# Performance work log

Measured on AMD Instinct MI355X. Metric: run time of the kernel, lower is better.

The kernel has to match this reference:

```python
import jax, jax.numpy as jnp
import numpy as np

B, NX, NY, NZ, C, MAX_PTS = 4, 512, 512, 1, 64, 32
P_PER_B = 16384            # non-empty pillars per frame (unique cells)
MASK_RATIO = 0.7


def setup_inputs() -> dict:
    key = jax.random.key(0)
    kf, kn, ks, kc = jax.random.split(key, 4)
    grid = NZ * NX * NY
    # unique linear pillar locations per batch element -> deterministic scatter-set
    lin = jnp.stack([
        jax.random.permutation(jax.random.fold_in(kc, b), grid)[:P_PER_B]
        for b in range(B)
    ])  # [B, P]
    y = (lin // NX).reshape(-1)
    x = (lin % NX).reshape(-1)
    bidx = jnp.repeat(jnp.arange(B), P_PER_B)
    voxel_coords = jnp.stack(
        [bidx, jnp.zeros_like(bidx), y, x], axis=1).astype(jnp.int32)  # [M,4] = (b,z,y,x)
    M = B * P_PER_B
    pillar_features = jax.random.normal(kf, (M, C), dtype=jnp.float32)
    voxel_num_points = jax.random.randint(kn, (M,), 1, MAX_PTS + 1, dtype=jnp.int32)
    K = int(M * (1.0 - MASK_RATIO))
    select_index = jnp.sort(jax.random.permutation(ks, M)[:K]).astype(jnp.int32)
    return {
        "pillar_features": pillar_features,
        "voxel_coords": voxel_coords,
        "voxel_num_points": voxel_num_points,
        "select_index": select_index,
    }


def reference(pillar_features, voxel_coords, voxel_num_points, select_index):
    grid = NZ * NX * NY
    # per-pillar flat index into the batched dense grid:
    # within-frame index = z + y*nx + x (nz == 1), offset by batch*grid
    flat = (voxel_coords[:, 0] * grid
            + voxel_coords[:, 1]
            + voxel_coords[:, 2] * NX
            + voxel_coords[:, 3])  # [M]

    fdt = pillar_features.dtype
    occupancy = jnp.zeros(B * grid, dtype=fdt).at[flat].set(1.0).reshape(B, NY, NX)
    points_number = (jnp.zeros(B * grid, dtype=voxel_num_points.dtype)
                     .at[flat].set(voxel_num_points).reshape(B, NY, NX))
    density = (jnp.zeros(B * grid, dtype=fdt)
               .at[flat].set(voxel_num_points.astype(fdt) / MAX_PTS)
               .reshape(B, NY, NX))

    # scatter only the unmasked (selected) pillar features into the dense BEV grid
    flat_sel = flat[select_index]               # [K]
    feats_sel = pillar_features[select_index]   # [K, C]
    spatial = (jnp.zeros((B * grid, C), dtype=fdt)
               .at[flat_sel].set(feats_sel)
               .reshape(B, grid, C)
               .transpose(0, 2, 1)
               .reshape(B, C * NZ, NY, NX))
    return spatial, occupancy, density, points_number
```

## Files before the change

kernel.cpp:

```cpp
#include <hip/hip_runtime.h>

#define NXD   512
#define NYD   512
#define CD    64
#define BD    4
#define GRIDC (NXD * NYD)

__global__ void scatter_meta_kernel(const int* __restrict__ coords,
                                    const int* __restrict__ npts,
                                    float* __restrict__ occ,
                                    float* __restrict__ dens,
                                    float* __restrict__ pnum,
                                    int M) {
    int i = blockIdx.x * blockDim.x + threadIdx.x;
    if (i >= M) return;
    int b = coords[4 * i + 0];
    int z = coords[4 * i + 1];
    int y = coords[4 * i + 2];
    int x = coords[4 * i + 3];
    int cell = b * GRIDC + z + y * NXD + x;
    float n = (float)npts[i];
    occ[cell]  = 1.0f;
    dens[cell] = n * (1.0f / 32.0f);
    pnum[cell] = n;
}

__global__ void scatter_spatial_kernel(const float* __restrict__ feats,
                                       const int* __restrict__ coords,
                                       const int* __restrict__ sel,
                                       float* __restrict__ spatial,
                                       int K) {
    int group = blockIdx.x * (blockDim.x >> 6) + (threadIdx.x >> 6);
    int c     = threadIdx.x & 63;
    if (group >= K) return;
    int row = sel[group];
    int b = coords[4 * row + 0];
    int z = coords[4 * row + 1];
    int y = coords[4 * row + 2];
    int x = coords[4 * row + 3];
    int cell = z + y * NXD + x;
    float v = feats[(size_t)row * CD + c];
    spatial[(size_t)b * ((size_t)CD * GRIDC) + (size_t)c * GRIDC + (size_t)cell] = v;
}

extern "C" void kernel_launch(void* const* d_in, const int* in_sizes, int n_in,
                              void* d_out, int out_size, void* d_ws, size_t ws_size,
                              hipStream_t stream) {
    const float* feats  = (const float*)d_in[0];
    const int*   coords = (const int*)d_in[1];
    const int*   npts   = (const int*)d_in[2];
    const int*   sel    = (const int*)d_in[3];

    int M = in_sizes[2];
    int K = in_sizes[3];

    float* out = (float*)d_out;
    size_t spatial_elems = (size_t)BD * CD * GRIDC;
    size_t map_elems     = (size_t)BD * GRIDC;
    float* occ  = out + spatial_elems;
    float* dens = occ + map_elems;
    float* pnum = dens + map_elems;

    hipMemsetAsync(d_out, 0, (size_t)out_size * sizeof(float), stream);

    scatter_meta_kernel<<<(M + 255) / 256, 256, 0, stream>>>(
        coords, npts, occ, dens, pnum, M);

    scatter_spatial_kernel<<<(K + 3) / 4, 256, 0, stream>>>(
        feats, coords, sel, out, K);
}
```

Baseline: 68.91 us.

## Replace memset-plus-scatter with cell-map build and fused dense gather fill

Builds a per-cell index map in workspace using atomics that encode the pillar row and a selected flag. A single fused kernel then writes every spatial, occupancy, density and point-count element exactly once, gathering features through the map and using nontemporal vector stores. This removes the separate full-output memset and the scattered strided writes. In exchange it adds a map memset and build kernel, scattered feature reads, and depends on sufficient workspace.

```diff
diff --git a/kernel.cpp b/kernel.cpp
--- a/kernel.cpp
+++ b/kernel.cpp
@@ -5,6 +5,89 @@
 #define CD    64
 #define BD    4
 #define GRIDC (NXD * NYD)
+#define SEL_FLAG (1 << 20)
+
+typedef float f32x4 __attribute__((ext_vector_type(4)));
+typedef int   i32x4 __attribute__((ext_vector_type(4)));
+
+
+__global__ void build_map_kernel(const int* __restrict__ coords,
+                                 const int* __restrict__ sel,
+                                 int* __restrict__ map, int M, int K) {
+    int i = blockIdx.x * blockDim.x + threadIdx.x;
+    if (i < M) {
+        int b = coords[4 * i + 0];
+        int z = coords[4 * i + 1];
+        int y = coords[4 * i + 2];
+        int x = coords[4 * i + 3];
+        int cell = b * GRIDC + z + y * NXD + x;
+        atomicOr(map + cell, i + 1);
+    } else if (i < M + K) {
+        int r = sel[i - M];
+        int b = coords[4 * r + 0];
+        int z = coords[4 * r + 1];
+        int y = coords[4 * r + 2];
+        int x = coords[4 * r + 3];
+        int cell = b * GRIDC + z + y * NXD + x;
+        atomicOr(map + cell, SEL_FLAG);
+    }
+}
+
+__global__ __launch_bounds__(256) void fused_fill_kernel(
+        const float* __restrict__ feats,
+        const int*   __restrict__ npts,
+        const int*   __restrict__ map,
+        float* __restrict__ out) {
+    const size_t base = (size_t)blockIdx.x * 1024;
+    const int b   = (int)(base >> 18);
+    const int cif = (int)(base & (GRIDC - 1));
+    const int t   = threadIdx.x;
+    const size_t cbase = base + (size_t)t * 4;
+
+    const i32x4 m4 = *reinterpret_cast<const i32x4*>(map + cbase);
+    int rows[4] = {m4.x, m4.y, m4.z, m4.w};
+
+    float* __restrict__ spatial = out;
+    const size_t sp_off = (size_t)b * ((size_t)CD * GRIDC) + (size_t)(cif + t * 4);
+
+    #pragma unroll 4
+    for (int c = 0; c < CD; ++c) {
+        f32x4 v = (f32x4)(0.f);
+        #pragma unroll
+        for (int j = 0; j < 4; ++j) {
+            int m = rows[j];
+            if (m & SEL_FLAG)
+                v[j] = feats[(size_t)((m & 0xFFFFF) - 1) * CD + c];
+        }
+        __builtin_nontemporal_store(
+            v, reinterpret_cast<f32x4*>(spatial + sp_off + (size_t)c * GRIDC));
+    }
+
+    const size_t spatial_elems = (size_t)BD * CD * GRIDC;
+    const size_t map_elems     = (size_t)BD * GRIDC;
+    float* __restrict__ occ  = out + spatial_elems;
+    float* __restrict__ dens = occ + map_elems;
+    float* __restrict__ pnum = dens + map_elems;
+
+    f32x4 o, d, p;
+    #pragma unroll
+    for (int j = 0; j < 4; ++j) {
+        int m = rows[j];
+        if (m != 0) {
+            int row = (m & 0xFFFFF) - 1;
+            float n = (float)npts[row];
+            o[j] = 1.0f;
+            d[j] = n * (1.0f / 32.0f);
+            p[j] = n;
+        } else {
+            o[j] = 0.f; d[j] = 0.f; p[j] = 0.f;
+        }
+    }
+    __builtin_nontemporal_store(o, reinterpret_cast<f32x4*>(occ  + cbase));
+    __builtin_nontemporal_store(d, reinterpret_cast<f32x4*>(dens + cbase));
+    __builtin_nontemporal_store(p, reinterpret_cast<f32x4*>(pnum + cbase));
+}
+
 
 __global__ void scatter_meta_kernel(const int* __restrict__ coords,
                                     const int* __restrict__ npts,
@@ -51,21 +134,29 @@
     const int*   npts   = (const int*)d_in[2];
     const int*   sel    = (const int*)d_in[3];
 
-    int M = in_sizes[2];
-    int K = in_sizes[3];
+    const int M = in_sizes[2];
+    const int K = in_sizes[3];
 
     float* out = (float*)d_out;
-    size_t spatial_elems = (size_t)BD * CD * GRIDC;
-    size_t map_elems     = (size_t)BD * GRIDC;
-    float* occ  = out + spatial_elems;
-    float* dens = occ + map_elems;
-    float* pnum = dens + map_elems;
+    const size_t map_bytes = (size_t)BD * GRIDC * sizeof(int);
 
-    hipMemsetAsync(d_out, 0, (size_t)out_size * sizeof(float), stream);
-
-    scatter_meta_kernel<<<(M + 255) / 256, 256, 0, stream>>>(
-        coords, npts, occ, dens, pnum, M);
-
-    scatter_spatial_kernel<<<(K + 3) / 4, 256, 0, stream>>>(
-        feats, coords, sel, out, K);
+    if (ws_size >= map_bytes) {
+        int* map = (int*)d_ws;
+        (void)hipMemsetAsync(map, 0, map_bytes, stream);
+        build_map_kernel<<<(M + K + 255) / 256, 256, 0, stream>>>(
+            coords, sel, map, M, K);
+        fused_fill_kernel<<<(BD * GRIDC) / 1024, 256, 0, stream>>>(
+            feats, npts, map, out);
+    } else {
+        size_t spatial_elems = (size_t)BD * CD * GRIDC;
+        size_t map_elems     = (size_t)BD * GRIDC;
+        float* occ  = out + spatial_elems;
+        float* dens = occ + map_elems;
+        float* pnum = dens + map_elems;
+        (void)hipMemsetAsync(d_out, 0, (size_t)out_size * sizeof(float), stream);
+        scatter_meta_kernel<<<(M + 255) / 256, 256, 0, stream>>>(
+            coords, npts, occ, dens, pnum, M);
+        scatter_spatial_kernel<<<(K + 3) / 4, 256, 0, stream>>>(
+            feats, coords, sel, out, K);
+    }
 }
```

Result: no change. 68.85 us (-0.1%).
